# Kernel tuning notes

Measured on AMD Instinct MI355X. Metric: run time of the kernel, lower is better.

## Reference

```python
import jax, jax.numpy as jnp
import numpy as np
import math

D = 1024
B, S = 4, 4096


def setup_inputs() -> dict:
    key = jax.random.key(0)
    ks = jax.random.split(key, 8)
    x = jax.random.normal(ks[0], (B, S, D), dtype=jnp.float32)
    W_omega = jax.random.normal(ks[1], (D, D), dtype=jnp.float32) * (1.0 / math.sqrt(D))
    b_omega = jnp.zeros((D,), dtype=jnp.float32)
    log_scale = jnp.full((D,), math.log(0.1), dtype=jnp.float32)
    ln_gamma = jnp.ones((4 * D,), dtype=jnp.float32)
    ln_beta = jnp.zeros((4 * D,), dtype=jnp.float32)
    W1 = jax.random.normal(ks[2], (4 * D, 2 * D), dtype=jnp.float32) * (1.0 / math.sqrt(4 * D))
    b1 = jnp.zeros((2 * D,), dtype=jnp.float32)
    W2 = jax.random.normal(ks[3], (2 * D, D), dtype=jnp.float32) * (1.0 / math.sqrt(2 * D))
    b2 = jnp.zeros((D,), dtype=jnp.float32)
    return {"x": x, "W_omega": W_omega, "b_omega": b_omega, "log_scale": log_scale,
            "ln_gamma": ln_gamma, "ln_beta": ln_beta, "W1": W1, "b1": b1, "W2": W2, "b2": b2}


def _layernorm(x, gamma, beta, eps=1e-5):
    mu = jnp.mean(x, axis=-1, keepdims=True)
    var = jnp.var(x, axis=-1, keepdims=True)
    return (x - mu) * jax.lax.rsqrt(var + eps) * gamma + beta


def reference(x, W_omega, b_omega, log_scale, ln_gamma, ln_beta, W1, b1, W2, b2):
    # x: (B, S, D)
    seq_len = x.shape[1]
    omega = jnp.einsum('bsd,de->bse', x, W_omega) + b_omega
    position = jnp.arange(1, seq_len + 1, dtype=x.dtype)[None, :, None]  # (1,S,1)
    pos_scale = 1.0 / jnp.sqrt(position)
    scale = jnp.exp(log_scale)
    omega_scaled = omega * scale * pos_scale
    phi = jnp.cumsum(omega_scaled, axis=1)
    cos_phi = jnp.cos(phi)
    sin_phi = jnp.sin(phi)
    content_real = x * cos_phi
    content_imag = x * sin_phi
    mem_real = jnp.cumsum(content_real, axis=1) / position
    mem_imag = jnp.cumsum(content_imag, axis=1) / position
    retrieved_real = mem_real * cos_phi + mem_imag * sin_phi
    retrieved_imag = mem_imag * cos_phi - mem_real * sin_phi
    context = jnp.concatenate([content_real, content_imag, retrieved_real, retrieved_imag], axis=-1)
    h = _layernorm(context, ln_gamma, ln_beta)
    h = jnp.einsum('bsf,fg->bsg', h, W1) + b1
    h = jax.nn.gelu(h, approximate=False)  # torch GELU default is exact erf
    # dropout is identity in eval mode
    phase_contribution = jnp.einsum('bsg,gd->bsd', h, W2) + b2
    return x + phase_contribution
```

## Files before the change

### kernel.cpp

```cpp
#include <hip/hip_runtime.h>
#include <hip/hip_bf16.h>
#include <math.h>

typedef __hip_bfloat16 bf16;
typedef __attribute__((ext_vector_type(8))) short bf16x8;
typedef __attribute__((ext_vector_type(4))) float f32x4;

static constexpr int DD = 1024;
static constexpr int BB = 4;
static constexpr int SS = 4096;
static constexpr int FD = 4096;
static constexpr int GDIM = 2048;
static constexpr long SD = (long)SS * DD;
static constexpr long SD4 = 4 * SD;

__device__ __forceinline__ void gl2lds16(const bf16* g, bf16* l) {
    __builtin_amdgcn_global_load_lds(
        (const __attribute__((address_space(1))) void*)g,
        (__attribute__((address_space(3))) void*)l, 16, 0, 0);
}

template <int EPI>
__global__ __launch_bounds__(256, EPI == 1 ? 4 : 1) void gemm_bt(
    const bf16* __restrict__ A, const bf16* __restrict__ BT, void* __restrict__ Cp,
    const float* __restrict__ bias, const float* __restrict__ Xadd,
    int M, int N, int K, long strA, long strBT, long strC)
{
    __shared__ __align__(16) bf16 As[128 * 32];
    __shared__ __align__(16) bf16 Bs[128 * 32];
    const int t = threadIdx.x;
    const int l = t & 63, wv = t >> 6;

    const int lin = blockIdx.y * gridDim.x + blockIdx.x;
    const int per = gridDim.x << 3;
    const int p = lin / per, r = lin - p * per;
    const long m0 = (long)(p * 8 + (r & 7)) * 128;
    const long n0 = (long)(r >> 3) * 128;

    A += (long)blockIdx.z * strA;
    BT += (long)blockIdx.z * strBT;

    const int rowOff = wv * 16 + (l >> 2);
    const int kgrp = (l & 3) ^ ((l >> 2) & 3);
    const bf16* pa = A + (m0 + rowOff) * (long)K + kgrp * 8;
    const bf16* pa2 = pa + 64L * K;
    const bf16* pb = BT + (n0 + rowOff) * (long)K + kgrp * 8;
    const bf16* pb2 = pb + 64L * K;
    bf16* la = &As[(wv * 16) * 32];
    bf16* la2 = &As[(wv * 16 + 64) * 32];
    bf16* lb = &Bs[(wv * 16) * 32];
    bf16* lb2 = &Bs[(wv * 16 + 64) * 32];

    f32x4 acc[4][4];
#pragma unroll
    for (int i = 0; i < 4; i++)
#pragma unroll
        for (int j = 0; j < 4; j++) acc[i][j] = (f32x4){0.f, 0.f, 0.f, 0.f};

    const int wr = wv >> 1, wc = wv & 1;
    const int fm = l & 15, q = l >> 4;
    const int sw = (q ^ (fm & 3)) << 3;

    for (int k0 = 0; k0 < K; k0 += 32) {
        gl2lds16(pa, la);
        gl2lds16(pa2, la2);
        gl2lds16(pb, lb);
        gl2lds16(pb2, lb2);
        pa += 32; pa2 += 32; pb += 32; pb2 += 32;
        __syncthreads();
        bf16x8 af[4], bfr[4];
#pragma unroll
        for (int i = 0; i < 4; i++)
            af[i] = *(const bf16x8*)&As[(wr * 64 + i * 16 + fm) * 32 + sw];
#pragma unroll
        for (int j = 0; j < 4; j++)
            bfr[j] = *(const bf16x8*)&Bs[(wc * 64 + j * 16 + fm) * 32 + sw];
#pragma unroll
        for (int i = 0; i < 4; i++)
#pragma unroll
            for (int j = 0; j < 4; j++)
                acc[i][j] = __builtin_amdgcn_mfma_f32_16x16x32_bf16(af[i], bfr[j], acc[i][j], 0, 0, 0);
        __syncthreads();
    }

    const long cb = (long)blockIdx.z * strC;
#pragma unroll
    for (int i = 0; i < 4; i++) {
#pragma unroll
        for (int j = 0; j < 4; j++) {
            const long col = n0 + wc * 64 + j * 16 + fm;
            const long rB = m0 + wr * 64 + i * 16 + q * 4;
#pragma unroll
            for (int r2 = 0; r2 < 4; r2++) {
                const long row = rB + r2;
                float v = acc[i][j][r2];
                if (EPI == 0) {
                    v += bias[row];
                    ((bf16*)Cp)[cb + row * (long)N + col] = __float2bfloat16(v);
                } else if (EPI == 1) {
                    v += bias[col];
                    v = 0.5f * v * (1.0f + erff(v * 0.70710678118654752f));
                    ((bf16*)Cp)[cb + row * (long)N + col] = __float2bfloat16(v);
                } else {
                    v += bias[col] + Xadd[row * (long)N + col];
                    ((float*)Cp)[cb + row * (long)N + col] = v;
                }
            }
        }
    }
}

__global__ void conv_bf16(const float* __restrict__ in, bf16* __restrict__ out, long n) {
    long i = ((long)blockIdx.x * 256 + threadIdx.x) * 4;
    if (i >= n) return;
    const float4 v = *(const float4*)(in + i);
    bf16 o[4] = {__float2bfloat16(v.x), __float2bfloat16(v.y),
                 __float2bfloat16(v.z), __float2bfloat16(v.w)};
    *(uint2*)(out + i) = *(uint2*)o;
}

__global__ void transpose_f32_bf16(const float* __restrict__ in, bf16* __restrict__ out,
                                   int R, int C, long inStr, long outStr) {
    __shared__ float tl[64][65];
    const float* ip = in + (long)blockIdx.z * inStr;
    bf16* op = out + (long)blockIdx.z * outStr;
    const int r0 = blockIdx.y * 64, c0 = blockIdx.x * 64;
    const int tr = threadIdx.x >> 6, tc = threadIdx.x & 63;
#pragma unroll
    for (int k = 0; k < 16; k++) {
        int r = k * 4 + tr;
        tl[r][tc] = ip[(long)(r0 + r) * C + c0 + tc];
    }
    __syncthreads();
#pragma unroll
    for (int k = 0; k < 16; k++) {
        int r = k * 4 + tr;
        op[(long)(c0 + r) * R + r0 + tc] = __float2bfloat16(tl[tc][r]);
    }
}

__global__ __launch_bounds__(256) void scan_kernel(
    const bf16* __restrict__ omegaT, const bf16* __restrict__ xT,
    const float* __restrict__ log_scale, bf16* __restrict__ ctx,
    long strIn, long strCtx)
{
    const int d = blockIdx.x * 4 + (threadIdx.x >> 6);
    const int lane = threadIdx.x & 63;
    const float sc = expf(log_scale[d]);
    const bf16* po = omegaT + (long)blockIdx.z * strIn + (long)d * SS;
    const bf16* px = xT + (long)blockIdx.z * strIn + (long)d * SS;
    bf16* pc = ctx + (long)blockIdx.z * strCtx + (long)d * SS;

    float phi_c = 0.f, mr_c = 0.f, mi_c = 0.f;
    for (int tchunk = 0; tchunk < SS / 64; tchunk++) {
        const int s = tchunk * 64 + lane;
        const float pos = (float)(s + 1);
        float w = __bfloat162float(po[s]) * sc * rsqrtf(pos);
#pragma unroll
        for (int dlt = 1; dlt < 64; dlt <<= 1) {
            float v = __shfl_up(w, dlt, 64);
            if (lane >= dlt) w += v;
        }
        const float phi = phi_c + w;
        float sph, cph;
        sincosf(phi, &sph, &cph);
        const float xv = __bfloat162float(px[s]);
        const float cr = xv * cph, ci = xv * sph;
        float crs = cr, cis = ci;
#pragma unroll
        for (int dlt = 1; dlt < 64; dlt <<= 1) {
            float v1 = __shfl_up(crs, dlt, 64);
            float v2 = __shfl_up(cis, dlt, 64);
            if (lane >= dlt) { crs += v1; cis += v2; }
        }
        const float invp = 1.0f / pos;
        const float mr = (mr_c + crs) * invp;
        const float mi = (mi_c + cis) * invp;
        const float rr = mr * cph + mi * sph;
        const float ri = mi * cph - mr * sph;
        pc[s] = __float2bfloat16(cr);
        pc[(long)DD * SS + s] = __float2bfloat16(ci);
        pc[2L * DD * SS + s] = __float2bfloat16(rr);
        pc[3L * DD * SS + s] = __float2bfloat16(ri);
        phi_c += __shfl(w, 63, 64);
        mr_c += __shfl(crs, 63, 64);
        mi_c += __shfl(cis, 63, 64);
    }
}

__global__ void zero_f32(float* p, int n) {
    int i = blockIdx.x * 256 + threadIdx.x;
    if (i < n) p[i] = 0.f;
}

__global__ void stats_kernel(const bf16* __restrict__ ctx, float* __restrict__ sums,
                             float* __restrict__ sqs) {
    const int s = blockIdx.x * 256 + threadIdx.x;
    const int f0 = blockIdx.y * 512;
    const int z = blockIdx.z;
    const bf16* p = ctx + (long)z * SD4 + (long)f0 * SS + s;
    float sm = 0.f, sq = 0.f;
    for (int f = 0; f < 512; f++) {
        float v = __bfloat162float(p[(long)f * SS]);
        sm += v;
        sq += v * v;
    }
    atomicAdd(&sums[z * SS + s], sm);
    atomicAdd(&sqs[z * SS + s], sq);
}

__global__ __launch_bounds__(256) void lnt_pair(
    bf16* __restrict__ ctx, const float* __restrict__ sums, const float* __restrict__ sqs,
    const float* __restrict__ gamma, const float* __restrict__ beta)
{
    __shared__ float tA[64][65];
    __shared__ float tB[64][65];
    const int z = blockIdx.z;
    int rem = blockIdx.x, a = 0;
    for (int i = 0; i < 64; i++) {
        int cnt = 64 - i;
        if (rem < cnt) { a = i; break; }
        rem -= cnt;
    }
    const int b = a + rem;
    bf16* base = ctx + (long)z * SD4;
    const int tr = threadIdx.x >> 6, tc = threadIdx.x & 63;
    const float* sums_z = sums + z * SS;
    const float* sqs_z = sqs + z * SS;

#pragma unroll
    for (int k = 0; k < 16; k++) {
        int i = k * 4 + tr;
        tA[i][tc] = __bfloat162float(base[(long)(a * 64 + i) * SS + b * 64 + tc]);
    }
    if (a != b) {
#pragma unroll
        for (int k = 0; k < 16; k++) {
            int i = k * 4 + tr;
            tB[i][tc] = __bfloat162float(base[(long)(b * 64 + i) * SS + a * 64 + tc]);
        }
    }
    __syncthreads();

    {
        const float g = gamma[a * 64 + tc], be = beta[a * 64 + tc];
#pragma unroll
        for (int k = 0; k < 16; k++) {
            const int i = k * 4 + tr;
            const int s = b * 64 + i;
            const float mu = sums_z[s] * (1.0f / FD);
            const float var = sqs_z[s] * (1.0f / FD) - mu * mu;
            const float is = rsqrtf(var + 1e-5f);
            const float v = (tA[tc][i] - mu) * is * g + be;
            base[(long)s * FD + a * 64 + tc] = __float2bfloat16(v);
        }
    }
    if (a != b) {
        const float g = gamma[b * 64 + tc], be = beta[b * 64 + tc];
#pragma unroll
        for (int k = 0; k < 16; k++) {
            const int i = k * 4 + tr;
            const int s = a * 64 + i;
            const float mu = sums_z[s] * (1.0f / FD);
            const float var = sqs_z[s] * (1.0f / FD) - mu * mu;
            const float is = rsqrtf(var + 1e-5f);
            const float v = (tB[tc][i] - mu) * is * g + be;
            base[(long)s * FD + b * 64 + tc] = __float2bfloat16(v);
        }
    }
}

extern "C" void kernel_launch(void* const* d_in, const int* in_sizes, int n_in,
                              void* d_out, int out_size, void* d_ws, size_t ws_size,
                              hipStream_t stream)
{
    const float* x = (const float*)d_in[0];
    const float* Wo = (const float*)d_in[1];
    const float* bo = (const float*)d_in[2];
    const float* lsc = (const float*)d_in[3];
    const float* gam = (const float*)d_in[4];
    const float* bet = (const float*)d_in[5];
    const float* W1 = (const float*)d_in[6];
    const float* b1 = (const float*)d_in[7];
    const float* W2 = (const float*)d_in[8];
    const float* b2 = (const float*)d_in[9];

    char* ws = (char*)d_ws;
    const size_t MB = 1024 * 1024;

    bf16* W1T = (bf16*)(ws + 0);
    bf16* W2T = (bf16*)(ws + 16 * MB);
    bf16* WoT = (bf16*)(ws + 20 * MB);
    float* sums = (float*)(ws + 22 * MB);
    float* sqs = sums + 4 * SS;

    transpose_f32_bf16<<<dim3(DD / 64, DD / 64, 1), 256, 0, stream>>>(Wo, WoT, DD, DD, 0, 0);
    transpose_f32_bf16<<<dim3(GDIM / 64, FD / 64, 1), 256, 0, stream>>>(W1, W1T, FD, GDIM, 0, 0);
    transpose_f32_bf16<<<dim3(DD / 64, GDIM / 64, 1), 256, 0, stream>>>(W2, W2T, GDIM, DD, 0, 0);

    const int NPAIR = 64 * 65 / 2;

    if (ws_size >= 220 * MB) {
        bf16* xT  = (bf16*)(ws + 23 * MB);
        bf16* omT = (bf16*)(ws + 55 * MB);
        bf16* ctx = (bf16*)(ws + 87 * MB);
        bf16* xb  = (bf16*)(ws + 87 * MB);
        bf16* h1  = (bf16*)(ws + 23 * MB);

        conv_bf16<<<(int)(BB * SD / 1024), 256, 0, stream>>>(x, xb, BB * SD);
        transpose_f32_bf16<<<dim3(DD / 64, SS / 64, BB), 256, 0, stream>>>(x, xT, SS, DD, SD, SD);

        gemm_bt<0><<<dim3(SS / 128, DD / 128, BB), 256, 0, stream>>>(
            WoT, xb, omT, bo, nullptr, DD, SS, DD, 0L, SD, SD);

        scan_kernel<<<dim3(DD / 4, 1, BB), 256, 0, stream>>>(omT, xT, lsc, ctx, SD, SD4);

        zero_f32<<<(8 * SS + 255) / 256, 256, 0, stream>>>(sums, 8 * SS);
        stats_kernel<<<dim3(SS / 256, FD / 512, BB), 256, 0, stream>>>(ctx, sums, sqs);

        lnt_pair<<<dim3(NPAIR, 1, BB), 256, 0, stream>>>(ctx, sums, sqs, gam, bet);

        gemm_bt<1><<<dim3(GDIM / 128, BB * SS / 128, 1), 256, 0, stream>>>(
            ctx, W1T, h1, b1, nullptr, BB * SS, GDIM, FD, 0L, 0L, 0L);

        gemm_bt<2><<<dim3(DD / 128, BB * SS / 128, 1), 256, 0, stream>>>(
            h1, W2T, d_out, b2, x, BB * SS, DD, GDIM, 0L, 0L, 0L);
    } else {
        bf16* xb  = (bf16*)(ws + 23 * MB);
        bf16* ctx = (bf16*)(ws + 23 * MB);
        bf16* omT = (bf16*)(ws + 55 * MB);
        bf16* xT  = (bf16*)(ws + 63 * MB);
        bf16* h1  = (bf16*)(ws + 55 * MB);

        for (int b = 0; b < BB; b++) {
            const float* xbf = x + (long)b * SD;
            conv_bf16<<<(int)(SD / 1024), 256, 0, stream>>>(xbf, xb, SD);
            transpose_f32_bf16<<<dim3(DD / 64, SS / 64, 1), 256, 0, stream>>>(xbf, xT, SS, DD, 0, 0);
            gemm_bt<0><<<dim3(SS / 128, DD / 128, 1), 256, 0, stream>>>(
                WoT, xb, omT, bo, nullptr, DD, SS, DD, 0L, 0L, 0L);
            scan_kernel<<<dim3(DD / 4, 1, 1), 256, 0, stream>>>(omT, xT, lsc, ctx, 0L, 0L);
            zero_f32<<<(2 * SS + 255) / 256, 256, 0, stream>>>(sums, 2 * SS);
            stats_kernel<<<dim3(SS / 256, FD / 512, 1), 256, 0, stream>>>(ctx, sums, sqs);
            lnt_pair<<<dim3(NPAIR, 1, 1), 256, 0, stream>>>(ctx, sums, sqs, gam, bet);
            gemm_bt<1><<<dim3(GDIM / 128, SS / 128, 1), 256, 0, stream>>>(
                ctx, W1T, h1, b1, nullptr, SS, GDIM, FD, 0L, 0L, 0L);
            gemm_bt<2><<<dim3(DD / 128, SS / 128, 1), 256, 0, stream>>>(
                h1, W2T, (float*)d_out + (long)b * SD, b2, xbf, SS, DD, GDIM, 0L, 0L, 0L);
        }
    }
}
```

Baseline: 850.1 us.

## Replace 128x128 GEMM with double-buffered 256x256 tile, 512 threads, XCD remap

All three GEMMs move to a new kernel with 256x256 output tiles, 8 waves and 64-deep K steps. Global-to-LDS loads are double-buffered and split into four interleaved phases, with barriers, explicit waitcnts and raised wave priority around the MFMA blocks. Workgroup IDs are remapped so neighbouring tiles land on the same XCD. The aim is better operand reuse per tile and overlap of memory loads with matrix math. The cost is 128KB of dynamic LDS and large accumulator register use, which limits occupancy.

```diff
diff --git a/kernel.cpp b/kernel.cpp
--- a/kernel.cpp
+++ b/kernel.cpp
@@ -21,77 +21,162 @@
 }
 
 template <int EPI>
-__global__ __launch_bounds__(256, EPI == 1 ? 4 : 1) void gemm_bt(
+__global__ __launch_bounds__(512, 2) void gemm256(
     const bf16* __restrict__ A, const bf16* __restrict__ BT, void* __restrict__ Cp,
     const float* __restrict__ bias, const float* __restrict__ Xadd,
     int M, int N, int K, long strA, long strBT, long strC)
 {
-    __shared__ __align__(16) bf16 As[128 * 32];
-    __shared__ __align__(16) bf16 Bs[128 * 32];
-    const int t = threadIdx.x;
-    const int l = t & 63, wv = t >> 6;
-
-    const int lin = blockIdx.y * gridDim.x + blockIdx.x;
-    const int per = gridDim.x << 3;
-    const int p = lin / per, r = lin - p * per;
-    const long m0 = (long)(p * 8 + (r & 7)) * 128;
-    const long n0 = (long)(r >> 3) * 128;
+    extern __shared__ bf16 lds[];
+    const int tid = threadIdx.x;
+    const int l = tid & 63, wv = tid >> 6;
+    const int wr = wv >> 2, wc = wv & 3;
+
+    int lin = blockIdx.y * gridDim.x + blockIdx.x;
+    {
+        const int nwg = gridDim.x * gridDim.y;
+        const int qq = nwg >> 3, rr = nwg & 7;
+        const int xcd = lin & 7, idx = lin >> 3;
+        lin = (xcd < rr ? xcd * (qq + 1) : rr * (qq + 1) + (xcd - rr) * qq) + idx;
+    }
+    const long m0 = (long)(lin / gridDim.x) * 256;
+    const long n0 = (long)(lin % gridDim.x) * 256;
 
     A += (long)blockIdx.z * strA;
     BT += (long)blockIdx.z * strBT;
 
-    const int rowOff = wv * 16 + (l >> 2);
-    const int kgrp = (l & 3) ^ ((l >> 2) & 3);
-    const bf16* pa = A + (m0 + rowOff) * (long)K + kgrp * 8;
-    const bf16* pa2 = pa + 64L * K;
-    const bf16* pb = BT + (n0 + rowOff) * (long)K + kgrp * 8;
-    const bf16* pb2 = pb + 64L * K;
-    bf16* la = &As[(wv * 16) * 32];
-    bf16* la2 = &As[(wv * 16 + 64) * 32];
-    bf16* lb = &Bs[(wv * 16) * 32];
-    bf16* lb2 = &Bs[(wv * 16 + 64) * 32];
-
-    f32x4 acc[4][4];
-#pragma unroll
-    for (int i = 0; i < 4; i++)
-#pragma unroll
-        for (int j = 0; j < 4; j++) acc[i][j] = (f32x4){0.f, 0.f, 0.f, 0.f};
-
-    const int wr = wv >> 1, wc = wv & 1;
+    const int schunk = (tid & 3) ^ ((tid >> 3) & 3);
+    const bf16* pa = A + (m0 + (tid >> 2)) * (long)K + schunk * 8;
+    const bf16* pb = BT + (n0 + (tid >> 2)) * (long)K + schunk * 8;
+    const long rowK = 128L * (long)K;
+    const int stgOff = wv * 512;
+
     const int fm = l & 15, q = l >> 4;
-    const int sw = (q ^ (fm & 3)) << 3;
-
-    for (int k0 = 0; k0 < K; k0 += 32) {
-        gl2lds16(pa, la);
-        gl2lds16(pa2, la2);
-        gl2lds16(pb, lb);
-        gl2lds16(pb2, lb2);
-        pa += 32; pa2 += 32; pb += 32; pb2 += 32;
-        __syncthreads();
-        bf16x8 af[4], bfr[4];
-#pragma unroll
-        for (int i = 0; i < 4; i++)
-            af[i] = *(const bf16x8*)&As[(wr * 64 + i * 16 + fm) * 32 + sw];
-#pragma unroll
-        for (int j = 0; j < 4; j++)
-            bfr[j] = *(const bf16x8*)&Bs[(wc * 64 + j * 16 + fm) * 32 + sw];
-#pragma unroll
-        for (int i = 0; i < 4; i++)
-#pragma unroll
-            for (int j = 0; j < 4; j++)
-                acc[i][j] = __builtin_amdgcn_mfma_f32_16x16x32_bf16(af[i], bfr[j], acc[i][j], 0, 0, 0);
-        __syncthreads();
+    const int lof = fm * 32 + ((q ^ ((fm >> 1) & 3)) * 8);
+
+    f32x4 acc[8][4];
+#pragma unroll
+    for (int i = 0; i < 8; ++i)
+#pragma unroll
+        for (int j = 0; j < 4; ++j) acc[i][j] = (f32x4){0.f, 0.f, 0.f, 0.f};
+
+    const int NT = K >> 6;
+
+    {
+        bf16* dA0 = lds + stgOff;
+        bf16* dB0 = lds + 32768 + stgOff;
+        bf16* dA1 = lds + 8192 + stgOff;
+        bf16* dB1 = lds + 40960 + stgOff;
+        gl2lds16(pa, dA0);       gl2lds16(pa + rowK, dA0 + 4096);
+        gl2lds16(pb, dB0);       gl2lds16(pb + rowK, dB0 + 4096);
+        gl2lds16(pa + 32, dA1);  gl2lds16(pa + 32 + rowK, dA1 + 4096);
+        gl2lds16(pb + 32, dB1);  gl2lds16(pb + 32 + rowK, dB1 + 4096);
+        asm volatile("s_waitcnt vmcnt(4)" ::: "memory");
+        __builtin_amdgcn_s_barrier();
+    }
+
+    bf16x8 af[4], bq[4];
+    for (int t = 0; t < NT; ++t) {
+        const int buf = t & 1;
+        const bool more = (t + 1) < NT;
+        const long ko = (long)(t + 1) * 64;
+        const bf16* As0 = lds + (buf << 1) * 8192;
+        const bf16* As1 = As0 + 8192;
+        const bf16* Bs0 = lds + 32768 + (buf << 1) * 8192;
+        const bf16* Bs1 = Bs0 + 8192;
+        bf16* nA0 = lds + ((buf ^ 1) << 1) * 8192 + stgOff;
+        bf16* nA1 = nA0 + 8192;
+        bf16* nB0 = lds + 32768 + ((buf ^ 1) << 1) * 8192 + stgOff;
+        bf16* nB1 = nB0 + 8192;
+
+        {
+            const bf16* bb = Bs0 + (wc * 64) * 32 + lof;
+            const bf16* ab = As0 + (wr * 128) * 32 + lof;
+#pragma unroll
+            for (int j = 0; j < 4; ++j) bq[j] = *(const bf16x8*)(bb + j * 512);
+#pragma unroll
+            for (int i = 0; i < 4; ++i) af[i] = *(const bf16x8*)(ab + i * 512);
+            if (more) { gl2lds16(pa + ko, nA0); gl2lds16(pa + ko + rowK, nA0 + 4096); }
+            __builtin_amdgcn_s_barrier();
+            asm volatile("s_waitcnt lgkmcnt(0)" ::: "memory");
+            __builtin_amdgcn_s_setprio(1);
+#pragma unroll
+            for (int i = 0; i < 4; ++i)
+#pragma unroll
+                for (int j = 0; j < 4; ++j)
+                    acc[i][j] = __builtin_amdgcn_mfma_f32_16x16x32_bf16(af[i], bq[j], acc[i][j], 0, 0, 0);
+            __builtin_amdgcn_s_setprio(0);
+            __builtin_amdgcn_s_barrier();
+        }
+        {
+            const bf16* ab = As0 + (wr * 128 + 64) * 32 + lof;
+#pragma unroll
+            for (int i = 0; i < 4; ++i) af[i] = *(const bf16x8*)(ab + i * 512);
+            if (more) {
+                gl2lds16(pb + ko, nB0); gl2lds16(pb + ko + rowK, nB0 + 4096);
+                asm volatile("s_waitcnt vmcnt(4)" ::: "memory");
+            } else {
+                asm volatile("s_waitcnt vmcnt(0)" ::: "memory");
+            }
+            __builtin_amdgcn_s_barrier();
+            asm volatile("s_waitcnt lgkmcnt(0)" ::: "memory");
+            __builtin_amdgcn_s_setprio(1);
+#pragma unroll
+            for (int i = 0; i < 4; ++i)
+#pragma unroll
+                for (int j = 0; j < 4; ++j)
+                    acc[4 + i][j] = __builtin_amdgcn_mfma_f32_16x16x32_bf16(af[i], bq[j], acc[4 + i][j], 0, 0, 0);
+            __builtin_amdgcn_s_setprio(0);
+            __builtin_amdgcn_s_barrier();
+        }
+        {
+            const bf16* bb = Bs1 + (wc * 64) * 32 + lof;
+            const bf16* ab = As1 + (wr * 128) * 32 + lof;
+#pragma unroll
+            for (int j = 0; j < 4; ++j) bq[j] = *(const bf16x8*)(bb + j * 512);
+#pragma unroll
+            for (int i = 0; i < 4; ++i) af[i] = *(const bf16x8*)(ab + i * 512);
+            if (more) { gl2lds16(pa + ko + 32, nA1); gl2lds16(pa + ko + 32 + rowK, nA1 + 4096); }
+            __builtin_amdgcn_s_barrier();
+            asm volatile("s_waitcnt lgkmcnt(0)" ::: "memory");
+            __builtin_amdgcn_s_setprio(1);
+#pragma unroll
+            for (int i = 0; i < 4; ++i)
+#pragma unroll
+                for (int j = 0; j < 4; ++j)
+                    acc[i][j] = __builtin_amdgcn_mfma_f32_16x16x32_bf16(af[i], bq[j], acc[i][j], 0, 0, 0);
+            __builtin_amdgcn_s_setprio(0);
+            __builtin_amdgcn_s_barrier();
+        }
+        {
+            const bf16* ab = As1 + (wr * 128 + 64) * 32 + lof;
+#pragma unroll
+            for (int i = 0; i < 4; ++i) af[i] = *(const bf16x8*)(ab + i * 512);
+            if (more) {
+                gl2lds16(pb + ko + 32, nB1); gl2lds16(pb + ko + 32 + rowK, nB1 + 4096);
+                asm volatile("s_waitcnt vmcnt(4)" ::: "memory");
+            }
+            __builtin_amdgcn_s_barrier();
+            asm volatile("s_waitcnt lgkmcnt(0)" ::: "memory");
+            __builtin_amdgcn_s_setprio(1);
+#pragma unroll
+            for (int i = 0; i < 4; ++i)
+#pragma unroll
+                for (int j = 0; j < 4; ++j)
+                    acc[4 + i][j] = __builtin_amdgcn_mfma_f32_16x16x32_bf16(af[i], bq[j], acc[4 + i][j], 0, 0, 0);
+            __builtin_amdgcn_s_setprio(0);
+            __builtin_amdgcn_s_barrier();
+        }
     }
 
     const long cb = (long)blockIdx.z * strC;
 #pragma unroll
-    for (int i = 0; i < 4; i++) {
-#pragma unroll
-        for (int j = 0; j < 4; j++) {
+    for (int i = 0; i < 8; ++i) {
+        const long rB = m0 + wr * 128 + i * 16 + q * 4;
+#pragma unroll
+        for (int j = 0; j < 4; ++j) {
             const long col = n0 + wc * 64 + j * 16 + fm;
-            const long rB = m0 + wr * 64 + i * 16 + q * 4;
-#pragma unroll
-            for (int r2 = 0; r2 < 4; r2++) {
+#pragma unroll
+            for (int r2 = 0; r2 < 4; ++r2) {
                 const long row = rB + r2;
                 float v = acc[i][j][r2];
                 if (EPI == 0) {
@@ -285,6 +370,17 @@
     const float* W2 = (const float*)d_in[8];
     const float* b2 = (const float*)d_in[9];
 
+    static bool attr_done = false;
+    if (!attr_done) {
+        hipFuncSetAttribute(reinterpret_cast<const void*>(gemm256<0>),
+                            hipFuncAttributeMaxDynamicSharedMemorySize, 131072);
+        hipFuncSetAttribute(reinterpret_cast<const void*>(gemm256<1>),
+                            hipFuncAttributeMaxDynamicSharedMemorySize, 131072);
+        hipFuncSetAttribute(reinterpret_cast<const void*>(gemm256<2>),
+                            hipFuncAttributeMaxDynamicSharedMemorySize, 131072);
+        attr_done = true;
+    }
+
     char* ws = (char*)d_ws;
     const size_t MB = 1024 * 1024;
 
@@ -310,7 +406,7 @@
         conv_bf16<<<(int)(BB * SD / 1024), 256, 0, stream>>>(x, xb, BB * SD);
         transpose_f32_bf16<<<dim3(DD / 64, SS / 64, BB), 256, 0, stream>>>(x, xT, SS, DD, SD, SD);
 
-        gemm_bt<0><<<dim3(SS / 128, DD / 128, BB), 256, 0, stream>>>(
+        gemm256<0><<<dim3(SS / 256, DD / 256, BB), 512, 131072, stream>>>(
             WoT, xb, omT, bo, nullptr, DD, SS, DD, 0L, SD, SD);
 
         scan_kernel<<<dim3(DD / 4, 1, BB), 256, 0, stream>>>(omT, xT, lsc, ctx, SD, SD4);
@@ -320,10 +416,10 @@
 
         lnt_pair<<<dim3(NPAIR, 1, BB), 256, 0, stream>>>(ctx, sums, sqs, gam, bet);
 
-        gemm_bt<1><<<dim3(GDIM / 128, BB * SS / 128, 1), 256, 0, stream>>>(
+        gemm256<1><<<dim3(GDIM / 256, BB * SS / 256, 1), 512, 131072, stream>>>(
             ctx, W1T, h1, b1, nullptr, BB * SS, GDIM, FD, 0L, 0L, 0L);
 
-        gemm_bt<2><<<dim3(DD / 128, BB * SS / 128, 1), 256, 0, stream>>>(
+        gemm256<2><<<dim3(DD / 256, BB * SS / 256, 1), 512, 131072, stream>>>(
             h1, W2T, d_out, b2, x, BB * SS, DD, GDIM, 0L, 0L, 0L);
     } else {
         bf16* xb  = (bf16*)(ws + 23 * MB);
@@ -336,15 +432,15 @@
             const float* xbf = x + (long)b * SD;
             conv_bf16<<<(int)(SD / 1024), 256, 0, stream>>>(xbf, xb, SD);
             transpose_f32_bf16<<<dim3(DD / 64, SS / 64, 1), 256, 0, stream>>>(xbf, xT, SS, DD, 0, 0);
-            gemm_bt<0><<<dim3(SS / 128, DD / 128, 1), 256, 0, stream>>>(
+            gemm256<0><<<dim3(SS / 256, DD / 256, 1), 512, 131072, stream>>>(
                 WoT, xb, omT, bo, nullptr, DD, SS, DD, 0L, 0L, 0L);
             scan_kernel<<<dim3(DD / 4, 1, 1), 256, 0, stream>>>(omT, xT, lsc, ctx, 0L, 0L);
             zero_f32<<<(2 * SS + 255) / 256, 256, 0, stream>>>(sums, 2 * SS);
             stats_kernel<<<dim3(SS / 256, FD / 512, 1), 256, 0, stream>>>(ctx, sums, sqs);
             lnt_pair<<<dim3(NPAIR, 1, 1), 256, 0, stream>>>(ctx, sums, sqs, gam, bet);
-            gemm_bt<1><<<dim3(GDIM / 128, SS / 128, 1), 256, 0, stream>>>(
+            gemm256<1><<<dim3(GDIM / 256, SS / 256, 1), 512, 131072, stream>>>(
                 ctx, W1T, h1, b1, nullptr, SS, GDIM, FD, 0L, 0L, 0L);
-            gemm_bt<2><<<dim3(DD / 128, SS / 128, 1), 256, 0, stream>>>(
+            gemm256<2><<<dim3(DD / 256, SS / 256, 1), 512, 131072, stream>>>(
                 h1, W2T, (float*)d_out + (long)b * SD, b2, xbf, SS, DD, GDIM, 0L, 0L, 0L);
         }
     }
```

Measured after the change: 732.4 us. 1.16x faster.
